# Kernel optimization log

Measured on AMD Instinct MI355X. Metric: run time of the kernel, lower is better.

## Reference

```python
import jax, jax.numpy as jnp
import numpy as np


def _reduce1(x):
    # x: [B, n, d] -> [B, 2d]; exists=max, forall=min over objects (exclude_self is a no-op for cnt=1)
    return jnp.concatenate([x.max(axis=1), x.min(axis=1)], axis=-1)


def _reduce2(x):
    # x: [B, n, n, d] -> [B, n, 2d]; exclude_self masks diagonal i==j (0 for exists/max, 1 for forall/min)
    n = x.shape[1]
    diag = jnp.eye(n, dtype=bool)[None, :, :, None]
    exists = jnp.where(diag, 0.0, x).max(axis=2)
    forall = jnp.where(diag, 1.0, x).min(axis=2)
    return jnp.concatenate([exists, forall], axis=-1)


def _layer(f0, f1, f2, p):
    # One LogicLayer step (breadth=2, minmax reducer, exclude_self, sigmoid norm, no hidden layers)
    W0, b0, W1, b1, W2, b2 = p
    B, n, d1 = f1.shape
    # order 0: [self, reduce(order1)]
    g0 = jnp.concatenate([f0, _reduce1(f1)], axis=-1)
    o0 = jax.nn.sigmoid(g0 @ W0 + b0)
    # order 1: [expand(order0), self, reduce(order2)]
    e0 = jnp.broadcast_to(f0[:, None, :], (B, n, f0.shape[-1]))
    g1 = jnp.concatenate([e0, f1, _reduce2(f2)], axis=-1)
    o1 = jax.nn.sigmoid(g1 @ W1 + b1)
    # order 2: [expand(order1), self] then Permutation(2) = cat(x, swap(i,j))
    e1 = jnp.broadcast_to(f1[:, :, None, :], (B, n, n, d1))
    g2 = jnp.concatenate([e1, f2], axis=-1)
    g2 = jnp.concatenate([g2, jnp.swapaxes(g2, 1, 2)], axis=-1)
    o2 = jax.nn.sigmoid(g2 @ W2 + b2)
    return o0, o1, o2


def setup_inputs() -> dict:
    key = jax.random.key(0)
    B, n = 4, 256
    d = [32, 64, 64]
    O = 128
    ks = iter(jax.random.split(key, 64))
    inp = {
        "x0": jax.random.uniform(next(ks), (B, d[0]), dtype=jnp.float32),
        "x1": jax.random.uniform(next(ks), (B, n, d[1]), dtype=jnp.float32),
        "x2": jax.random.uniform(next(ks), (B, n, n, d[2]), dtype=jnp.float32),
    }
    fan_ins = [
        (d[0] + 2 * d[1], d[0] + d[1] + 2 * d[2], 2 * (d[1] + d[2])),  # layer 0
        (O + 2 * O, O + O + 2 * O, 2 * (O + O)),                        # layer 1
        (O + 2 * O, O + O + 2 * O, 2 * (O + O)),                        # layer 2
    ]
    for l, fins in enumerate(fan_ins):
        for o, fin in enumerate(fins):
            inp[f"W{o}_{l}"] = jax.random.normal(next(ks), (fin, O), dtype=jnp.float32) / np.sqrt(fin).astype(np.float32)
            inp[f"b{o}_{l}"] = jnp.zeros((O,), dtype=jnp.float32)
    return inp


def reference(x0, x1, x2,
              W0_0, b0_0, W1_0, b1_0, W2_0, b2_0,
              W0_1, b0_1, W1_1, b1_1, W2_1, b2_1,
              W0_2, b0_2, W1_2, b1_2, W2_2, b2_2):
    f = (x0, x1, x2)
    for p in ((W0_0, b0_0, W1_0, b1_0, W2_0, b2_0),
              (W0_1, b0_1, W1_1, b1_1, W2_1, b2_1),
              (W0_2, b0_2, W1_2, b1_2, W2_2, b2_2)):
        f = _layer(*f, p)
    return f
```

## Files before the change

### kernel.cpp

```cpp
#include <hip/hip_runtime.h>
#include <hip/hip_bf16.h>
#include <cstdint>

#define NN 256
#define NB 4
#define OC 128

using bf16x8_t = __attribute__((ext_vector_type(8))) __bf16;
using f32x4_t  = __attribute__((ext_vector_type(4))) float;

typedef const __attribute__((address_space(1))) uint8_t* gptr1_t;
typedef __attribute__((address_space(3))) uint8_t* lptr3_t;

__device__ __forceinline__ void async_load16(const void* g, void* l) {
  __builtin_amdgcn_global_load_lds((gptr1_t)g, (lptr3_t)l, 16, 0, 0);
}

__device__ __forceinline__ float sigf(float x) {
  return 1.0f / (1.0f + __expf(-x));
}

__device__ __forceinline__ uint16_t f2bf_rne(float f) {
  uint32_t u = __float_as_uint(f);
  uint32_t r = (u + 0x7fffu + ((u >> 16) & 1u)) >> 16;
  return (uint16_t)r;
}

__device__ __forceinline__ void emit_wt(const float* __restrict__ W2,
                                        uint16_t* __restrict__ Wt, int d1,
                                        int d2, int idx) {
  const int K = 2 * d2;
  const int nn = idx / K, k = idx - nn * K;
  const int row = (k < d2) ? (d1 + k) : (2 * d1 + d2 + (k - d2));
  Wt[idx] = f2bf_rne(W2[row * OC + nn]);
}

__device__ __forceinline__ void emit_bt(const float* __restrict__ W1,
                                        const float* __restrict__ W2,
                                        uint16_t* __restrict__ Bt, int D0,
                                        int D1, int D2, int FIN1, int KP,
                                        int idx) {
  const int n = idx / KP, k = idx - n * KP;
  float val = 0.f;
  if (n < 128) {
    if (k < FIN1) val = W1[k * OC + n];
  } else if (n < 256) {
    if (k >= D0 && k < D0 + D1) val = W2[(k - D0) * OC + (n - 128)];
  } else {
    if (k >= D0 && k < D0 + D1) val = W2[(D1 + D2 + (k - D0)) * OC + (n - 256)];
  }
  Bt[idx] = f2bf_rne(val);
}

__global__ __launch_bounds__(256) void prep_all(
    const float* __restrict__ W2_0, const float* __restrict__ W2_1,
    const float* __restrict__ W2_2, const float* __restrict__ W1_0,
    const float* __restrict__ W1_1, const float* __restrict__ W1_2,
    const float* __restrict__ x0, const float* __restrict__ x1,
    uint16_t* __restrict__ Wt0, uint16_t* __restrict__ Wt1,
    uint16_t* __restrict__ Wt2, uint16_t* __restrict__ Bt0,
    uint16_t* __restrict__ Bt1, uint16_t* __restrict__ Bt2,
    uint16_t* __restrict__ g1bf0, float* __restrict__ r2b,
    float* __restrict__ r2c) {
  int g = blockIdx.x * 256 + threadIdx.x;
  if (g < 16384) { emit_wt(W2_0, Wt0, 64, 64, g); return; }
  g -= 16384;
  if (g < 32768) { emit_wt(W2_1, Wt1, 128, 128, g); return; }
  g -= 32768;
  if (g < 32768) { emit_wt(W2_2, Wt2, 128, 128, g); return; }
  g -= 32768;
  if (g < 98304) { emit_bt(W1_0, W2_0, Bt0, 32, 64, 64, 224, 256, g); return; }
  g -= 98304;
  if (g < 196608) { emit_bt(W1_1, W2_1, Bt1, 128, 128, 128, 512, 512, g); return; }
  g -= 196608;
  if (g < 196608) { emit_bt(W1_2, W2_2, Bt2, 128, 128, 128, 512, 512, g); return; }
  g -= 196608;
  if (g < 131072) {
    const int row = g >> 7, t = g & 127;
    uint16_t* const gp = g1bf0 + (size_t)row * 256;
    if (t < 32) gp[t] = f2bf_rne(x0[(row >> 8) * 32 + t]);
    else if (t < 96) gp[t] = f2bf_rne(x1[(size_t)row * 64 + (t - 32)]);
    else gp[128 + t] = 0;
    return;
  }
  g -= 131072;
  if (g < 262144) { r2b[g] = ((g & 255) < 128) ? 0.f : 1.f; return; }
  g -= 262144;
  if (g < 262144) { r2c[g] = ((g & 255) < 128) ? 0.f : 1.f; }
}

__global__ __launch_bounds__(256) void reduce2_l0_kernel(
    const float* __restrict__ x2, uint16_t* __restrict__ g1bf0,
    uint16_t* __restrict__ x2bf) {
  const int bid = blockIdx.x;
  const int i = bid & 255;
  const int tid = threadIdx.x;
  const int q = tid & 15, s = tid >> 4;
  const size_t rowbase = ((size_t)bid * NN) * 64 + q * 4;
  float mxA0 = 0.f, mxA1 = 0.f, mxA2 = 0.f, mxA3 = 0.f;
  float mnA0 = 1.f, mnA1 = 1.f, mnA2 = 1.f, mnA3 = 1.f;
  float mxB0 = 0.f, mxB1 = 0.f, mxB2 = 0.f, mxB3 = 0.f;
  float mnB0 = 1.f, mnB1 = 1.f, mnB2 = 1.f, mnB3 = 1.f;
#pragma unroll 2
  for (int t = 0; t < 16; t += 2) {
    const int jA = s + t * 16, jB = jA + 16;
    const float4 xa = *(const float4*)(x2 + rowbase + (size_t)jA * 64);
    const float4 xb = *(const float4*)(x2 + rowbase + (size_t)jB * 64);
    uint2 pa, pb;
    pa.x = (uint32_t)f2bf_rne(xa.x) | ((uint32_t)f2bf_rne(xa.y) << 16);
    pa.y = (uint32_t)f2bf_rne(xa.z) | ((uint32_t)f2bf_rne(xa.w) << 16);
    pb.x = (uint32_t)f2bf_rne(xb.x) | ((uint32_t)f2bf_rne(xb.y) << 16);
    pb.y = (uint32_t)f2bf_rne(xb.z) | ((uint32_t)f2bf_rne(xb.w) << 16);
    *(uint2*)(x2bf + rowbase + (size_t)jA * 64) = pa;
    *(uint2*)(x2bf + rowbase + (size_t)jB * 64) = pb;
    if (jA != i) {
      mxA0 = fmaxf(mxA0, xa.x); mxA1 = fmaxf(mxA1, xa.y);
      mxA2 = fmaxf(mxA2, xa.z); mxA3 = fmaxf(mxA3, xa.w);
      mnA0 = fminf(mnA0, xa.x); mnA1 = fminf(mnA1, xa.y);
      mnA2 = fminf(mnA2, xa.z); mnA3 = fminf(mnA3, xa.w);
    }
    if (jB != i) {
      mxB0 = fmaxf(mxB0, xb.x); mxB1 = fmaxf(mxB1, xb.y);
      mxB2 = fmaxf(mxB2, xb.z); mxB3 = fmaxf(mxB3, xb.w);
      mnB0 = fminf(mnB0, xb.x); mnB1 = fminf(mnB1, xb.y);
      mnB2 = fminf(mnB2, xb.z); mnB3 = fminf(mnB3, xb.w);
    }
  }
  float mx0 = fmaxf(mxA0, mxB0), mx1 = fmaxf(mxA1, mxB1);
  float mx2 = fmaxf(mxA2, mxB2), mx3 = fmaxf(mxA3, mxB3);
  float mn0 = fminf(mnA0, mnB0), mn1 = fminf(mnA1, mnB1);
  float mn2 = fminf(mnA2, mnB2), mn3 = fminf(mnA3, mnB3);
  __shared__ float4 smx[256], smn[256];
  smx[tid] = make_float4(mx0, mx1, mx2, mx3);
  smn[tid] = make_float4(mn0, mn1, mn2, mn3);
  __syncthreads();
  if (s == 0) {
    for (int ss = 1; ss < 16; ++ss) {
      float4 a = smx[q + ss * 16], c = smn[q + ss * 16];
      mx0 = fmaxf(mx0, a.x); mx1 = fmaxf(mx1, a.y);
      mx2 = fmaxf(mx2, a.z); mx3 = fmaxf(mx3, a.w);
      mn0 = fminf(mn0, c.x); mn1 = fminf(mn1, c.y);
      mn2 = fminf(mn2, c.z); mn3 = fminf(mn3, c.w);
    }
    uint16_t* const g = g1bf0 + (size_t)bid * 256;
    g[96 + q * 4 + 0] = f2bf_rne(mx0); g[96 + q * 4 + 1] = f2bf_rne(mx1);
    g[96 + q * 4 + 2] = f2bf_rne(mx2); g[96 + q * 4 + 3] = f2bf_rne(mx3);
    g[160 + q * 4 + 0] = f2bf_rne(mn0); g[160 + q * 4 + 1] = f2bf_rne(mn1);
    g[160 + q * 4 + 2] = f2bf_rne(mn2); g[160 + q * 4 + 3] = f2bf_rne(mn3);
  }
}

template <int KP, int D0, int D1, bool DUP>
__global__ __launch_bounds__(256) void small_gemm(
    const uint16_t* __restrict__ g1, const uint16_t* __restrict__ Bt,
    const float* __restrict__ b1, const float* __restrict__ b2,
    float* __restrict__ f1out, uint16_t* __restrict__ g1next,
    float* __restrict__ u, float* __restrict__ vT,
    const float* __restrict__ f0in, const float* __restrict__ f1in,
    const float* __restrict__ W0, const float* __restrict__ b0,
    float* __restrict__ f0out) {
  constexpr int NCH = KP / 64;
  const int bid = blockIdx.x;
  const int tid = threadIdx.x;

  __shared__ __align__(16) uint8_t ldsA[8192];
  __shared__ __align__(16) uint8_t ldsB[16384];

  if (bid < 48) {
    const int mt = bid / 3, nt = bid - mt * 3;
    const int m0 = mt * 64, n0 = nt * 128;
    const int wv = tid >> 6, lane = tid & 63;
    const int l15 = lane & 15, l4 = lane >> 4;

    f32x4_t acc[4][2];
#pragma unroll
    for (int a = 0; a < 4; ++a)
#pragma unroll
      for (int q = 0; q < 2; ++q) acc[a][q] = (f32x4_t){0.f, 0.f, 0.f, 0.f};

    for (int c = 0; c < NCH; ++c) {
      const int kbg = c * 64;
#pragma unroll
      for (int t = 0; t < 2; ++t) {
        const int id = wv * 2 + t;
        const int mi = id & 3, ks = id >> 2;
        async_load16(g1 + (size_t)(m0 + mi * 16 + l15) * KP + kbg + ks * 32 + l4 * 8,
                     ldsA + id * 1024);
      }
#pragma unroll
      for (int t = 0; t < 4; ++t) {
        const int id = wv * 4 + t;
        const int ni = id & 7, ks = id >> 3;
        async_load16(Bt + (size_t)(n0 + ni * 16 + l15) * KP + kbg + ks * 32 + l4 * 8,
                     ldsB + id * 1024);
      }
      __syncthreads();
#pragma unroll
      for (int ks = 0; ks < 2; ++ks) {
        bf16x8_t Af[4], Bf[2];
#pragma unroll
        for (int a = 0; a < 4; ++a)
          Af[a] = *(const bf16x8_t*)(ldsA + ((ks * 4 + a) << 10) + (lane << 4));
#pragma unroll
        for (int q = 0; q < 2; ++q)
          Bf[q] = *(const bf16x8_t*)(ldsB + ((ks * 8 + wv * 2 + q) << 10) + (lane << 4));
#pragma unroll
        for (int a = 0; a < 4; ++a)
#pragma unroll
          for (int q = 0; q < 2; ++q)
            acc[a][q] = __builtin_amdgcn_mfma_f32_16x16x32_bf16(Af[a], Bf[q],
                                                                acc[a][q], 0, 0, 0);
      }
      __syncthreads();
    }

    float bias[2];
#pragma unroll
    for (int q = 0; q < 2; ++q) {
      const int cc = wv * 32 + q * 16 + l15;
      bias[q] = (nt == 0) ? b1[cc] : ((nt == 1) ? b2[cc] : 0.f);
    }
#pragma unroll
    for (int a = 0; a < 4; ++a) {
      const int rl = a * 16 + l4 * 4;
#pragma unroll
      for (int r = 0; r < 4; ++r) {
        const size_t bi = m0 + rl + r;
#pragma unroll
        for (int q = 0; q < 2; ++q) {
          const int cc = wv * 32 + q * 16 + l15;
          const float x = acc[a][q][r] + bias[q];
          if (nt == 0) {
            const float val = sigf(x);
            f1out[bi * OC + cc] = val;
            if (DUP) g1next[bi * 512 + 128 + cc] = f2bf_rne(val);
          } else if (nt == 1) {
            u[bi * OC + cc] = x;
          } else {
            const int b = (int)(bi >> 8), j = (int)(bi & 255);
            vT[((size_t)b * OC + cc) * NN + j] = x;
          }
        }
      }
    }
  } else {
    constexpr int FIN0 = D0 + 2 * D1;
    constexpr int S = 256 / D1;
    const int b = bid - 48;
    float* const sm = (float*)ldsA;
    float* const g0 = sm;
    float* const smx = sm + 512;
    float* const smn = sm + 768;
    float* const sval = sm + 1024;
    const int cc = tid & (D1 - 1), ss = tid / D1;
    float mx = -1e30f, mn = 1e30f;
    const float* f1b = f1in + (size_t)b * NN * D1;
    for (int j = ss; j < NN; j += S) {
      const float x = f1b[(size_t)j * D1 + cc];
      mx = fmaxf(mx, x); mn = fminf(mn, x);
    }
    smx[tid] = mx; smn[tid] = mn;
    __syncthreads();
    if (ss == 0) {
      for (int s2 = 1; s2 < S; ++s2) {
        mx = fmaxf(mx, smx[cc + s2 * D1]);
        mn = fminf(mn, smn[cc + s2 * D1]);
      }
      g0[D0 + cc] = mx;
      g0[D0 + D1 + cc] = mn;
    }
    if (tid < D0) g0[tid] = f0in[b * D0 + tid];
    __syncthreads();
    if (tid < OC) {
      float acc = b0[tid];
#pragma unroll 8
      for (int k = 0; k < FIN0; ++k) acc += g0[k] * W0[k * OC + tid];
      const float val = sigf(acc);
      f0out[b * OC + tid] = val;
      sval[tid] = val;
    }
    if (DUP) {
      __syncthreads();
      for (int idx = tid; idx < 256 * 128; idx += 256) {
        const int row = idx >> 7, c2 = idx & 127;
        g1next[((size_t)(b * 256 + row)) * 512 + c2] = f2bf_rne(sval[c2]);
      }
    }
  }
}

__global__ __launch_bounds__(256) void conv_r2_kernel(
    const float* __restrict__ r2, uint16_t* __restrict__ g1next) {
  const int bi = blockIdx.x, t = threadIdx.x;
  g1next[(size_t)bi * 512 + 256 + t] = f2bf_rne(r2[(size_t)bi * 256 + t]);
}

template <int D2, typename OUT_T, bool REDUCE>
__global__ __launch_bounds__(256, 4) void gemm2_kernel(
    const __hip_bfloat16* __restrict__ f2, const uint16_t* __restrict__ Wt,
    const float* __restrict__ u, const float* __restrict__ vT,
    OUT_T* __restrict__ out, float* __restrict__ r2n) {
  constexpr int K = 2 * D2;
  constexpr int NCH = K / 64;
  constexpr bool BF16OUT = (sizeof(OUT_T) == 2);
  constexpr int LDSB = BF16OUT ? (128 * 272) : 32768;
  const int bid = blockIdx.x;
  const int jt = bid & 1, i = (bid >> 1) & 255, b = bid >> 9;
  const int j0 = jt * 128;
  const int tid = threadIdx.x;
  const int wv = tid >> 6, lane = tid & 63;
  const int wr = wv >> 1, wc = wv & 1;
  const int l15 = lane & 15, l4 = lane >> 4;

  __shared__ __align__(16) uint8_t lds[LDSB];
  __shared__ unsigned smax[128], smin[128];
  uint8_t* const ldsA = lds;
  uint8_t* const ldsW = lds + 16384;

  const __hip_bfloat16* A1 = f2 + ((size_t)(b * NN + i) * NN + j0) * D2;
  const __hip_bfloat16* A2 = f2 + ((size_t)(b * NN + j0) * NN + i) * D2;

  f32x4_t acc[4][4];
#pragma unroll
  for (int a = 0; a < 4; ++a)
#pragma unroll
    for (int q = 0; q < 4; ++q) acc[a][q] = (f32x4_t){0.f, 0.f, 0.f, 0.f};

  for (int c = 0; c < NCH; ++c) {
    const int kbg = c * 64;
    const bool second = (kbg >= D2);
    const __hip_bfloat16* Ab = second ? A2 : A1;
    const size_t rstride = second ? (size_t)NN * D2 : (size_t)D2;
    const int kbase = second ? (kbg - D2) : kbg;
#pragma unroll
    for (int q = 0; q < 4; ++q) {
      const int id = wv * 4 + q;
      const int mi = id & 7, ks = id >> 3;
      const int row = mi * 16 + l15;
      const int kk = ks * 32 + l4 * 8;
      async_load16(Ab + (size_t)row * rstride + kbase + kk, ldsA + id * 1024);
    }
#pragma unroll
    for (int q = 0; q < 4; ++q) {
      const int id = wv * 4 + q;
      const int ni = id & 7, ks = id >> 3;
      const int nn2 = ni * 16 + l15;
      const int kk = ks * 32 + l4 * 8;
      async_load16(Wt + (size_t)nn2 * K + kbg + kk, ldsW + id * 1024);
    }
    __syncthreads();
#pragma unroll
    for (int ks = 0; ks < 2; ++ks) {
      bf16x8_t Af[4], Bf[4];
#pragma unroll
      for (int a = 0; a < 4; ++a)
        Af[a] = *(const bf16x8_t*)(ldsA + ((ks * 8 + wr * 4 + a) << 10) + (lane << 4));
#pragma unroll
      for (int q = 0; q < 4; ++q)
        Bf[q] = *(const bf16x8_t*)(ldsW + ((ks * 8 + wc * 4 + q) << 10) + (lane << 4));
#pragma unroll
      for (int a = 0; a < 4; ++a)
#pragma unroll
        for (int q = 0; q < 4; ++q)
          acc[a][q] = __builtin_amdgcn_mfma_f32_16x16x32_bf16(Af[a], Bf[q],
                                                              acc[a][q], 0, 0, 0);
    }
    __syncthreads();
  }

  const size_t bi2 = (size_t)(b * NN + i);
  float uval[4];
#pragma unroll
  for (int q = 0; q < 4; ++q) uval[q] = u[bi2 * OC + wc * 64 + q * 16 + l15];
  const size_t obase = (bi2 * NN + j0) * OC;
  const float* const vTb = vT + (size_t)b * OC * NN;

  if (BF16OUT) {
    if (REDUCE && tid < 128) { smax[tid] = 0u; smin[tid] = 0x3f800000u; }
    __syncthreads();
    float lmx[4] = {0.f, 0.f, 0.f, 0.f};
    float lmn[4] = {1.f, 1.f, 1.f, 1.f};
#pragma unroll
    for (int a = 0; a < 4; ++a) {
      const int rowb = wr * 64 + a * 16 + l4 * 4;
      const int jg = j0 + rowb;
#pragma unroll
      for (int q = 0; q < 4; ++q) {
        const int col = wc * 64 + q * 16 + l15;
        const float4 vq = *(const float4*)(vTb + (size_t)col * NN + jg);
#pragma unroll
        for (int r = 0; r < 4; ++r) {
          const int j = rowb + r;
          const float x = acc[a][q][r] + uval[q] + ((const float*)&vq)[r];
          const float sg = sigf(x);
          *(uint16_t*)(lds + j * 272 + col * 2) = f2bf_rne(sg);
          if (REDUCE && (jg + r) != i) {
            lmx[q] = fmaxf(lmx[q], sg);
            lmn[q] = fminf(lmn[q], sg);
          }
        }
      }
    }
    if (REDUCE) {
#pragma unroll
      for (int q = 0; q < 4; ++q) {
        const int col = wc * 64 + q * 16 + l15;
        atomicMax(&smax[col], __float_as_uint(lmx[q]));
        atomicMin(&smin[col], __float_as_uint(lmn[q]));
      }
    }
    __syncthreads();
    uint16_t* const outp = (uint16_t*)out;
#pragma unroll
    for (int ci = 0; ci < 8; ++ci) {
      const int chunk = ci * 256 + tid;
      const int row = chunk >> 4, off = chunk & 15;
      const uint4 val = *(const uint4*)(lds + row * 272 + off * 16);
      *(uint4*)(outp + obase + (size_t)row * OC + off * 8) = val;
    }
    if (REDUCE && tid < 128) {
      unsigned* const r2u = (unsigned*)r2n;
      atomicMax(&r2u[bi2 * 256 + tid], smax[tid]);
      atomicMin(&r2u[bi2 * 256 + 128 + tid], smin[tid]);
    }
  } else {
    float* const outp = (float*)out;
#pragma unroll
    for (int a = 0; a < 4; ++a) {
      const int rowb = wr * 64 + a * 16 + l4 * 4;
      const int jg = j0 + rowb;
#pragma unroll
      for (int q = 0; q < 4; ++q) {
        const int col = wc * 64 + q * 16 + l15;
        const float4 vq = *(const float4*)(vTb + (size_t)col * NN + jg);
#pragma unroll
        for (int r = 0; r < 4; ++r) {
          const int j = rowb + r;
          const float x = acc[a][q][r] + uval[q] + ((const float*)&vq)[r];
          outp[obase + (size_t)j * OC + col] = sigf(x);
        }
      }
    }
  }
}

extern "C" void kernel_launch(void* const* d_in, const int* in_sizes, int n_in,
                              void* d_out, int out_size, void* d_ws,
                              size_t ws_size, hipStream_t stream) {
  const float* x0 = (const float*)d_in[0];
  const float* x1 = (const float*)d_in[1];
  const float* x2 = (const float*)d_in[2];
  const float *Wp[3][3], *bp[3][3];
  for (int l = 0; l < 3; ++l)
    for (int o = 0; o < 3; ++o) {
      Wp[l][o] = (const float*)d_in[3 + l * 6 + o * 2];
      bp[l][o] = (const float*)d_in[3 + l * 6 + o * 2 + 1];
    }

  const size_t F2E = (size_t)NB * NN * NN * OC;
  const size_t X2E = (size_t)NB * NN * NN * 64;

  uint8_t* ws = (uint8_t*)d_ws;
  size_t off = 0;
  auto carve = [&](size_t bytes) -> uint8_t* {
    uint8_t* p = ws + off;
    off += (bytes + 255) & ~(size_t)255;
    return p;
  };
  float* f0a = (float*)carve((size_t)NB * OC * 4);
  float* f0b = (float*)carve((size_t)NB * OC * 4);
  float* f1a = (float*)carve((size_t)NB * NN * OC * 4);
  float* f1b = (float*)carve((size_t)NB * NN * OC * 4);
  float* r2b = (float*)carve((size_t)NB * NN * 256 * 4);
  float* r2c = (float*)carve((size_t)NB * NN * 256 * 4);
  float* uu  = (float*)carve((size_t)NB * NN * OC * 4);
  float* vT  = (float*)carve((size_t)NB * OC * NN * 4);
  uint16_t* Wt0 = (uint16_t*)carve((size_t)OC * 128 * 2);
  uint16_t* Wt1 = (uint16_t*)carve((size_t)OC * 256 * 2);
  uint16_t* Wt2 = (uint16_t*)carve((size_t)OC * 256 * 2);
  uint16_t* Bt0 = (uint16_t*)carve((size_t)384 * 256 * 2);
  uint16_t* Bt1 = (uint16_t*)carve((size_t)384 * 512 * 2);
  uint16_t* Bt2 = (uint16_t*)carve((size_t)384 * 512 * 2);
  uint16_t* g1bf0 = (uint16_t*)carve((size_t)NB * NN * 256 * 2);
  uint16_t* g1bf1 = (uint16_t*)carve((size_t)NB * NN * 512 * 2);
  uint16_t* g1bf2 = (uint16_t*)carve((size_t)NB * NN * 512 * 2);
  __hip_bfloat16* f2a = (__hip_bfloat16*)carve(F2E * 2);

  __hip_bfloat16* f2b;
  uint16_t* x2bf;
  if (ws_size >= off + F2E * 2) {
    f2b = (__hip_bfloat16*)carve(F2E * 2);
    x2bf = (uint16_t*)f2b;
  } else {
    f2b = (__hip_bfloat16*)d_in[2];
    x2bf = (uint16_t*)carve(X2E * 2);
  }

  float* out_f0 = (float*)d_out;
  float* out_f1 = out_f0 + (size_t)NB * OC;
  float* out_f2 = out_f1 + (size_t)NB * NN * OC;

  prep_all<<<4800, 256, 0, stream>>>(Wp[0][2], Wp[1][2], Wp[2][2], Wp[0][1],
                                     Wp[1][1], Wp[2][1], x0, x1, Wt0, Wt1, Wt2,
                                     Bt0, Bt1, Bt2, g1bf0, r2b, r2c);
  reduce2_l0_kernel<<<NB * NN, 256, 0, stream>>>(x2, g1bf0, x2bf);

  small_gemm<256, 32, 64, true><<<52, 256, 0, stream>>>(
      g1bf0, Bt0, bp[0][1], bp[0][2], f1a, g1bf1, uu, vT, x0, x1, Wp[0][0],
      bp[0][0], f0a);
  gemm2_kernel<64, __hip_bfloat16, true><<<NB * NN * 2, 256, 0, stream>>>(
      (const __hip_bfloat16*)x2bf, Wt0, uu, vT, f2a, r2b);
  conv_r2_kernel<<<NB * NN, 256, 0, stream>>>(r2b, g1bf1);

  small_gemm<512, 128, 128, true><<<52, 256, 0, stream>>>(
      g1bf1, Bt1, bp[1][1], bp[1][2], f1b, g1bf2, uu, vT, f0a, f1a, Wp[1][0],
      bp[1][0], f0b);
  gemm2_kernel<128, __hip_bfloat16, true><<<NB * NN * 2, 256, 0, stream>>>(
      f2a, Wt1, uu, vT, f2b, r2c);
  conv_r2_kernel<<<NB * NN, 256, 0, stream>>>(r2c, g1bf2);

  small_gemm<512, 128, 128, false><<<52, 256, 0, stream>>>(
      g1bf2, Bt2, bp[2][1], bp[2][2], out_f1, nullptr, uu, vT, f0b, f1b,
      Wp[2][0], bp[2][0], out_f0);
  gemm2_kernel<128, float, false><<<NB * NN * 2, 256, 0, stream>>>(
      f2b, Wt2, uu, vT, out_f2, nullptr);
}
```

Baseline: 518.6 us.

## Load MFMA operands directly from global memory and merge the prep and reduce kernels

New measurement: 569.4 us. 9.8% more time.

```diff
diff --git a/kernel.cpp b/kernel.cpp
--- a/kernel.cpp
+++ b/kernel.cpp
@@ -9,15 +9,8 @@
 using bf16x8_t = __attribute__((ext_vector_type(8))) __bf16;
 using f32x4_t  = __attribute__((ext_vector_type(4))) float;
 
-typedef const __attribute__((address_space(1))) uint8_t* gptr1_t;
-typedef __attribute__((address_space(3))) uint8_t* lptr3_t;
-
-__device__ __forceinline__ void async_load16(const void* g, void* l) {
-  __builtin_amdgcn_global_load_lds((gptr1_t)g, (lptr3_t)l, 16, 0, 0);
-}
-
 __device__ __forceinline__ float sigf(float x) {
-  return 1.0f / (1.0f + __expf(-x));
+  return __builtin_amdgcn_rcpf(1.0f + __expf(-x));
 }
 
 __device__ __forceinline__ uint16_t f2bf_rne(float f) {
@@ -52,7 +45,7 @@
   Bt[idx] = f2bf_rne(val);
 }
 
-__global__ __launch_bounds__(256) void prep_all(
+__global__ __launch_bounds__(256) void prep_reduce(
     const float* __restrict__ W2_0, const float* __restrict__ W2_1,
     const float* __restrict__ W2_2, const float* __restrict__ W1_0,
     const float* __restrict__ W1_1, const float* __restrict__ W1_2,
@@ -61,40 +54,43 @@
     uint16_t* __restrict__ Wt2, uint16_t* __restrict__ Bt0,
     uint16_t* __restrict__ Bt1, uint16_t* __restrict__ Bt2,
     uint16_t* __restrict__ g1bf0, float* __restrict__ r2b,
-    float* __restrict__ r2c) {
-  int g = blockIdx.x * 256 + threadIdx.x;
-  if (g < 16384) { emit_wt(W2_0, Wt0, 64, 64, g); return; }
-  g -= 16384;
-  if (g < 32768) { emit_wt(W2_1, Wt1, 128, 128, g); return; }
-  g -= 32768;
-  if (g < 32768) { emit_wt(W2_2, Wt2, 128, 128, g); return; }
-  g -= 32768;
-  if (g < 98304) { emit_bt(W1_0, W2_0, Bt0, 32, 64, 64, 224, 256, g); return; }
-  g -= 98304;
-  if (g < 196608) { emit_bt(W1_1, W2_1, Bt1, 128, 128, 128, 512, 512, g); return; }
-  g -= 196608;
-  if (g < 196608) { emit_bt(W1_2, W2_2, Bt2, 128, 128, 128, 512, 512, g); return; }
-  g -= 196608;
-  if (g < 131072) {
-    const int row = g >> 7, t = g & 127;
-    uint16_t* const gp = g1bf0 + (size_t)row * 256;
-    if (t < 32) gp[t] = f2bf_rne(x0[(row >> 8) * 32 + t]);
-    else if (t < 96) gp[t] = f2bf_rne(x1[(size_t)row * 64 + (t - 32)]);
-    else gp[128 + t] = 0;
+    float* __restrict__ r2c, const float* __restrict__ x2,
+    uint16_t* __restrict__ x2bf) {
+  __shared__ float4 smx[256], smn[256];
+  const int blk = blockIdx.x;
+  const int tid = threadIdx.x;
+
+  if (blk < 4800) {
+    int g = blk * 256 + tid;
+    if (g < 16384) { emit_wt(W2_0, Wt0, 64, 64, g); return; }
+    g -= 16384;
+    if (g < 32768) { emit_wt(W2_1, Wt1, 128, 128, g); return; }
+    g -= 32768;
+    if (g < 32768) { emit_wt(W2_2, Wt2, 128, 128, g); return; }
+    g -= 32768;
+    if (g < 98304) { emit_bt(W1_0, W2_0, Bt0, 32, 64, 64, 224, 256, g); return; }
+    g -= 98304;
+    if (g < 196608) { emit_bt(W1_1, W2_1, Bt1, 128, 128, 128, 512, 512, g); return; }
+    g -= 196608;
+    if (g < 196608) { emit_bt(W1_2, W2_2, Bt2, 128, 128, 128, 512, 512, g); return; }
+    g -= 196608;
+    if (g < 131072) {
+      const int row = g >> 7, t = g & 127;
+      uint16_t* const gp = g1bf0 + (size_t)row * 256;
+      if (t < 32) gp[t] = f2bf_rne(x0[(row >> 8) * 32 + t]);
+      else if (t < 96) gp[t] = f2bf_rne(x1[(size_t)row * 64 + (t - 32)]);
+      else gp[128 + t] = 0;
+      return;
+    }
+    g -= 131072;
+    if (g < 262144) { r2b[g] = ((g & 255) < 128) ? 0.f : 1.f; return; }
+    g -= 262144;
+    if (g < 262144) { r2c[g] = ((g & 255) < 128) ? 0.f : 1.f; }
     return;
   }
-  g -= 131072;
-  if (g < 262144) { r2b[g] = ((g & 255) < 128) ? 0.f : 1.f; return; }
-  g -= 262144;
-  if (g < 262144) { r2c[g] = ((g & 255) < 128) ? 0.f : 1.f; }
-}
-
-__global__ __launch_bounds__(256) void reduce2_l0_kernel(
-    const float* __restrict__ x2, uint16_t* __restrict__ g1bf0,
-    uint16_t* __restrict__ x2bf) {
-  const int bid = blockIdx.x;
+
+  const int bid = blk - 4800;
   const int i = bid & 255;
-  const int tid = threadIdx.x;
   const int q = tid & 15, s = tid >> 4;
   const size_t rowbase = ((size_t)bid * NN) * 64 + q * 4;
   float mxA0 = 0.f, mxA1 = 0.f, mxA2 = 0.f, mxA3 = 0.f;
@@ -130,7 +126,6 @@
   float mx2 = fmaxf(mxA2, mxB2), mx3 = fmaxf(mxA3, mxB3);
   float mn0 = fminf(mnA0, mnB0), mn1 = fminf(mnA1, mnB1);
   float mn2 = fminf(mnA2, mnB2), mn3 = fminf(mnA3, mnB3);
-  __shared__ float4 smx[256], smn[256];
   smx[tid] = make_float4(mx0, mx1, mx2, mx3);
   smn[tid] = make_float4(mn0, mn1, mn2, mn3);
   __syncthreads();
@@ -159,12 +154,9 @@
     const float* __restrict__ f0in, const float* __restrict__ f1in,
     const float* __restrict__ W0, const float* __restrict__ b0,
     float* __restrict__ f0out) {
-  constexpr int NCH = KP / 64;
   const int bid = blockIdx.x;
   const int tid = threadIdx.x;
-
-  __shared__ __align__(16) uint8_t ldsA[8192];
-  __shared__ __align__(16) uint8_t ldsB[16384];
+  __shared__ float sm[1280];
 
   if (bid < 48) {
     const int mt = bid / 3, nt = bid - mt * 3;
@@ -172,46 +164,37 @@
     const int wv = tid >> 6, lane = tid & 63;
     const int l15 = lane & 15, l4 = lane >> 4;
 
+    const uint16_t* const Ag = g1 + (size_t)m0 * KP;
+    const uint16_t* const Bg = Bt + (size_t)n0 * KP;
+    uint32_t offA[4], offB[2];
+#pragma unroll
+    for (int a = 0; a < 4; ++a)
+      offA[a] = (uint32_t)(a * 16 + l15) * KP + l4 * 8;
+#pragma unroll
+    for (int q = 0; q < 2; ++q)
+      offB[q] = (uint32_t)(wv * 32 + q * 16 + l15) * KP + l4 * 8;
+
     f32x4_t acc[4][2];
 #pragma unroll
     for (int a = 0; a < 4; ++a)
 #pragma unroll
       for (int q = 0; q < 2; ++q) acc[a][q] = (f32x4_t){0.f, 0.f, 0.f, 0.f};
 
-    for (int c = 0; c < NCH; ++c) {
-      const int kbg = c * 64;
-#pragma unroll
-      for (int t = 0; t < 2; ++t) {
-        const int id = wv * 2 + t;
-        const int mi = id & 3, ks = id >> 2;
-        async_load16(g1 + (size_t)(m0 + mi * 16 + l15) * KP + kbg + ks * 32 + l4 * 8,
-                     ldsA + id * 1024);
-      }
-#pragma unroll
-      for (int t = 0; t < 4; ++t) {
-        const int id = wv * 4 + t;
-        const int ni = id & 7, ks = id >> 3;
-        async_load16(Bt + (size_t)(n0 + ni * 16 + l15) * KP + kbg + ks * 32 + l4 * 8,
-                     ldsB + id * 1024);
-      }
-      __syncthreads();
-#pragma unroll
-      for (int ks = 0; ks < 2; ++ks) {
-        bf16x8_t Af[4], Bf[2];
-#pragma unroll
-        for (int a = 0; a < 4; ++a)
-          Af[a] = *(const bf16x8_t*)(ldsA + ((ks * 4 + a) << 10) + (lane << 4));
+#pragma unroll
+    for (int kb = 0; kb < KP; kb += 32) {
+      bf16x8_t Af[4], Bf[2];
+#pragma unroll
+      for (int a = 0; a < 4; ++a)
+        Af[a] = *(const bf16x8_t*)(Ag + offA[a] + kb);
+#pragma unroll
+      for (int q = 0; q < 2; ++q)
+        Bf[q] = *(const bf16x8_t*)(Bg + offB[q] + kb);
+#pragma unroll
+      for (int a = 0; a < 4; ++a)
 #pragma unroll
         for (int q = 0; q < 2; ++q)
-          Bf[q] = *(const bf16x8_t*)(ldsB + ((ks * 8 + wv * 2 + q) << 10) + (lane << 4));
-#pragma unroll
-        for (int a = 0; a < 4; ++a)
-#pragma unroll
-          for (int q = 0; q < 2; ++q)
-            acc[a][q] = __builtin_amdgcn_mfma_f32_16x16x32_bf16(Af[a], Bf[q],
-                                                                acc[a][q], 0, 0, 0);
-      }
-      __syncthreads();
+          acc[a][q] = __builtin_amdgcn_mfma_f32_16x16x32_bf16(Af[a], Bf[q],
+                                                              acc[a][q], 0, 0, 0);
     }
 
     float bias[2];
@@ -247,7 +230,6 @@
     constexpr int FIN0 = D0 + 2 * D1;
     constexpr int S = 256 / D1;
     const int b = bid - 48;
-    float* const sm = (float*)ldsA;
     float* const g0 = sm;
     float* const smx = sm + 512;
     float* const smn = sm + 768;
@@ -301,9 +283,8 @@
     const float* __restrict__ u, const float* __restrict__ vT,
     OUT_T* __restrict__ out, float* __restrict__ r2n) {
   constexpr int K = 2 * D2;
-  constexpr int NCH = K / 64;
   constexpr bool BF16OUT = (sizeof(OUT_T) == 2);
-  constexpr int LDSB = BF16OUT ? (128 * 272) : 32768;
+  constexpr int LDSB = BF16OUT ? (128 * 272) : 16;
   const int bid = blockIdx.x;
   const int jt = bid & 1, i = (bid >> 1) & 255, b = bid >> 9;
   const int j0 = jt * 128;
@@ -314,11 +295,21 @@
 
   __shared__ __align__(16) uint8_t lds[LDSB];
   __shared__ unsigned smax[128], smin[128];
-  uint8_t* const ldsA = lds;
-  uint8_t* const ldsW = lds + 16384;
-
-  const __hip_bfloat16* A1 = f2 + ((size_t)(b * NN + i) * NN + j0) * D2;
-  const __hip_bfloat16* A2 = f2 + ((size_t)(b * NN + j0) * NN + i) * D2;
+
+  const __hip_bfloat16* const A1 = f2 + ((size_t)(b * NN + i) * NN + j0) * D2;
+  const __hip_bfloat16* const A2 = f2 + ((size_t)(b * NN + j0) * NN + i) * D2;
+  const __hip_bfloat16* const Wg = (const __hip_bfloat16*)Wt;
+
+  uint32_t offA1[4], offA2[4], offW[4];
+#pragma unroll
+  for (int a = 0; a < 4; ++a) {
+    const uint32_t row = wr * 64 + a * 16 + l15;
+    offA1[a] = row * (uint32_t)D2 + l4 * 8;
+    offA2[a] = row * (uint32_t)(NN * D2) + l4 * 8;
+  }
+#pragma unroll
+  for (int q = 0; q < 4; ++q)
+    offW[q] = (uint32_t)(wc * 64 + q * 16 + l15) * K + l4 * 8;
 
   f32x4_t acc[4][4];
 #pragma unroll
@@ -326,46 +317,27 @@
 #pragma unroll
     for (int q = 0; q < 4; ++q) acc[a][q] = (f32x4_t){0.f, 0.f, 0.f, 0.f};
 
-  for (int c = 0; c < NCH; ++c) {
-    const int kbg = c * 64;
-    const bool second = (kbg >= D2);
-    const __hip_bfloat16* Ab = second ? A2 : A1;
-    const size_t rstride = second ? (size_t)NN * D2 : (size_t)D2;
-    const int kbase = second ? (kbg - D2) : kbg;
-#pragma unroll
-    for (int q = 0; q < 4; ++q) {
-      const int id = wv * 4 + q;
-      const int mi = id & 7, ks = id >> 3;
-      const int row = mi * 16 + l15;
-      const int kk = ks * 32 + l4 * 8;
-      async_load16(Ab + (size_t)row * rstride + kbase + kk, ldsA + id * 1024);
-    }
-#pragma unroll
-    for (int q = 0; q < 4; ++q) {
-      const int id = wv * 4 + q;
-      const int ni = id & 7, ks = id >> 3;
-      const int nn2 = ni * 16 + l15;
-      const int kk = ks * 32 + l4 * 8;
-      async_load16(Wt + (size_t)nn2 * K + kbg + kk, ldsW + id * 1024);
-    }
-    __syncthreads();
-#pragma unroll
-    for (int ks = 0; ks < 2; ++ks) {
-      bf16x8_t Af[4], Bf[4];
+#pragma unroll
+  for (int kb = 0; kb < K; kb += 32) {
+    bf16x8_t Af[4], Bf[4];
+    if (kb < D2) {
 #pragma unroll
       for (int a = 0; a < 4; ++a)
-        Af[a] = *(const bf16x8_t*)(ldsA + ((ks * 8 + wr * 4 + a) << 10) + (lane << 4));
+        Af[a] = *(const bf16x8_t*)(A1 + offA1[a] + kb);
+    } else {
+#pragma unroll
+      for (int a = 0; a < 4; ++a)
+        Af[a] = *(const bf16x8_t*)(A2 + offA2[a] + (kb - D2));
+    }
+#pragma unroll
+    for (int q = 0; q < 4; ++q)
+      Bf[q] = *(const bf16x8_t*)(Wg + offW[q] + kb);
+#pragma unroll
+    for (int a = 0; a < 4; ++a)
 #pragma unroll
       for (int q = 0; q < 4; ++q)
-        Bf[q] = *(const bf16x8_t*)(ldsW + ((ks * 8 + wc * 4 + q) << 10) + (lane << 4));
-#pragma unroll
-      for (int a = 0; a < 4; ++a)
-#pragma unroll
-        for (int q = 0; q < 4; ++q)
-          acc[a][q] = __builtin_amdgcn_mfma_f32_16x16x32_bf16(Af[a], Bf[q],
-                                                              acc[a][q], 0, 0, 0);
-    }
-    __syncthreads();
+        acc[a][q] = __builtin_amdgcn_mfma_f32_16x16x32_bf16(Af[a], Bf[q],
+                                                            acc[a][q], 0, 0, 0);
   }
 
   const size_t bi2 = (size_t)(b * NN + i);
@@ -500,10 +472,9 @@
   float* out_f1 = out_f0 + (size_t)NB * OC;
   float* out_f2 = out_f1 + (size_t)NB * NN * OC;
 
-  prep_all<<<4800, 256, 0, stream>>>(Wp[0][2], Wp[1][2], Wp[2][2], Wp[0][1],
-                                     Wp[1][1], Wp[2][1], x0, x1, Wt0, Wt1, Wt2,
-                                     Bt0, Bt1, Bt2, g1bf0, r2b, r2c);
-  reduce2_l0_kernel<<<NB * NN, 256, 0, stream>>>(x2, g1bf0, x2bf);
+  prep_reduce<<<4800 + NB * NN, 256, 0, stream>>>(
+      Wp[0][2], Wp[1][2], Wp[2][2], Wp[0][1], Wp[1][1], Wp[2][1], x0, x1, Wt0,
+      Wt1, Wt2, Bt0, Bt1, Bt2, g1bf0, r2b, r2c, x2, x2bf);
 
   small_gemm<256, 32, 64, true><<<52, 256, 0, stream>>>(
       g1bf0, Bt0, bp[0][1], bp[0][2], f1a, g1bf1, uu, vT, x0, x1, Wp[0][0],
```

## Double-buffer gemm2 K-loop and merge prep and layer-0 reduce kernels

Applied to the files above, without the earlier changes.

Result: no change. 514.1 us (-0.9%).

```diff
diff --git a/kernel.cpp b/kernel.cpp
--- a/kernel.cpp
+++ b/kernel.cpp
@@ -17,7 +17,7 @@
 }
 
 __device__ __forceinline__ float sigf(float x) {
-  return 1.0f / (1.0f + __expf(-x));
+  return __builtin_amdgcn_rcpf(1.0f + __expf(-x));
 }
 
 __device__ __forceinline__ uint16_t f2bf_rne(float f) {
@@ -52,7 +52,7 @@
   Bt[idx] = f2bf_rne(val);
 }
 
-__global__ __launch_bounds__(256) void prep_all(
+__global__ __launch_bounds__(256) void prep_reduce(
     const float* __restrict__ W2_0, const float* __restrict__ W2_1,
     const float* __restrict__ W2_2, const float* __restrict__ W1_0,
     const float* __restrict__ W1_1, const float* __restrict__ W1_2,
@@ -61,40 +61,43 @@
     uint16_t* __restrict__ Wt2, uint16_t* __restrict__ Bt0,
     uint16_t* __restrict__ Bt1, uint16_t* __restrict__ Bt2,
     uint16_t* __restrict__ g1bf0, float* __restrict__ r2b,
-    float* __restrict__ r2c) {
-  int g = blockIdx.x * 256 + threadIdx.x;
-  if (g < 16384) { emit_wt(W2_0, Wt0, 64, 64, g); return; }
-  g -= 16384;
-  if (g < 32768) { emit_wt(W2_1, Wt1, 128, 128, g); return; }
-  g -= 32768;
-  if (g < 32768) { emit_wt(W2_2, Wt2, 128, 128, g); return; }
-  g -= 32768;
-  if (g < 98304) { emit_bt(W1_0, W2_0, Bt0, 32, 64, 64, 224, 256, g); return; }
-  g -= 98304;
-  if (g < 196608) { emit_bt(W1_1, W2_1, Bt1, 128, 128, 128, 512, 512, g); return; }
-  g -= 196608;
-  if (g < 196608) { emit_bt(W1_2, W2_2, Bt2, 128, 128, 128, 512, 512, g); return; }
-  g -= 196608;
-  if (g < 131072) {
-    const int row = g >> 7, t = g & 127;
-    uint16_t* const gp = g1bf0 + (size_t)row * 256;
-    if (t < 32) gp[t] = f2bf_rne(x0[(row >> 8) * 32 + t]);
-    else if (t < 96) gp[t] = f2bf_rne(x1[(size_t)row * 64 + (t - 32)]);
-    else gp[128 + t] = 0;
+    float* __restrict__ r2c, const float* __restrict__ x2,
+    uint16_t* __restrict__ x2bf) {
+  __shared__ float4 smx[256], smn[256];
+  const int blk = blockIdx.x;
+  const int tid = threadIdx.x;
+
+  if (blk < 4800) {
+    int g = blk * 256 + tid;
+    if (g < 16384) { emit_wt(W2_0, Wt0, 64, 64, g); return; }
+    g -= 16384;
+    if (g < 32768) { emit_wt(W2_1, Wt1, 128, 128, g); return; }
+    g -= 32768;
+    if (g < 32768) { emit_wt(W2_2, Wt2, 128, 128, g); return; }
+    g -= 32768;
+    if (g < 98304) { emit_bt(W1_0, W2_0, Bt0, 32, 64, 64, 224, 256, g); return; }
+    g -= 98304;
+    if (g < 196608) { emit_bt(W1_1, W2_1, Bt1, 128, 128, 128, 512, 512, g); return; }
+    g -= 196608;
+    if (g < 196608) { emit_bt(W1_2, W2_2, Bt2, 128, 128, 128, 512, 512, g); return; }
+    g -= 196608;
+    if (g < 131072) {
+      const int row = g >> 7, t = g & 127;
+      uint16_t* const gp = g1bf0 + (size_t)row * 256;
+      if (t < 32) gp[t] = f2bf_rne(x0[(row >> 8) * 32 + t]);
+      else if (t < 96) gp[t] = f2bf_rne(x1[(size_t)row * 64 + (t - 32)]);
+      else gp[128 + t] = 0;
+      return;
+    }
+    g -= 131072;
+    if (g < 262144) { r2b[g] = ((g & 255) < 128) ? 0.f : 1.f; return; }
+    g -= 262144;
+    if (g < 262144) { r2c[g] = ((g & 255) < 128) ? 0.f : 1.f; }
     return;
   }
-  g -= 131072;
-  if (g < 262144) { r2b[g] = ((g & 255) < 128) ? 0.f : 1.f; return; }
-  g -= 262144;
-  if (g < 262144) { r2c[g] = ((g & 255) < 128) ? 0.f : 1.f; }
-}
-
-__global__ __launch_bounds__(256) void reduce2_l0_kernel(
-    const float* __restrict__ x2, uint16_t* __restrict__ g1bf0,
-    uint16_t* __restrict__ x2bf) {
-  const int bid = blockIdx.x;
+
+  const int bid = blk - 4800;
   const int i = bid & 255;
-  const int tid = threadIdx.x;
   const int q = tid & 15, s = tid >> 4;
   const size_t rowbase = ((size_t)bid * NN) * 64 + q * 4;
   float mxA0 = 0.f, mxA1 = 0.f, mxA2 = 0.f, mxA3 = 0.f;
@@ -130,7 +133,6 @@
   float mx2 = fmaxf(mxA2, mxB2), mx3 = fmaxf(mxA3, mxB3);
   float mn0 = fminf(mnA0, mnB0), mn1 = fminf(mnA1, mnB1);
   float mn2 = fminf(mnA2, mnB2), mn3 = fminf(mnA3, mnB3);
-  __shared__ float4 smx[256], smn[256];
   smx[tid] = make_float4(mx0, mx1, mx2, mx3);
   smn[tid] = make_float4(mn0, mn1, mn2, mn3);
   __syncthreads();
@@ -301,7 +303,7 @@
     const float* __restrict__ u, const float* __restrict__ vT,
     OUT_T* __restrict__ out, float* __restrict__ r2n) {
   constexpr int K = 2 * D2;
-  constexpr int NCH = K / 64;
+  constexpr int NCH = K / 32;
   constexpr bool BF16OUT = (sizeof(OUT_T) == 2);
   constexpr int LDSB = BF16OUT ? (128 * 272) : 32768;
   const int bid = blockIdx.x;
@@ -314,11 +316,9 @@
 
   __shared__ __align__(16) uint8_t lds[LDSB];
   __shared__ unsigned smax[128], smin[128];
-  uint8_t* const ldsA = lds;
-  uint8_t* const ldsW = lds + 16384;
-
-  const __hip_bfloat16* A1 = f2 + ((size_t)(b * NN + i) * NN + j0) * D2;
-  const __hip_bfloat16* A2 = f2 + ((size_t)(b * NN + j0) * NN + i) * D2;
+
+  const __hip_bfloat16* const A1 = f2 + ((size_t)(b * NN + i) * NN + j0) * D2;
+  const __hip_bfloat16* const A2 = f2 + ((size_t)(b * NN + j0) * NN + i) * D2;
 
   f32x4_t acc[4][4];
 #pragma unroll
@@ -326,47 +326,66 @@
 #pragma unroll
     for (int q = 0; q < 4; ++q) acc[a][q] = (f32x4_t){0.f, 0.f, 0.f, 0.f};
 
-  for (int c = 0; c < NCH; ++c) {
-    const int kbg = c * 64;
+  auto STAGE = [&](int c, int buf) {
+    const int kbg = c * 32;
+    uint8_t* const bA = lds + buf * 16384;
+    uint8_t* const bW = bA + 8192;
     const bool second = (kbg >= D2);
-    const __hip_bfloat16* Ab = second ? A2 : A1;
+    const __hip_bfloat16* const Ab = second ? A2 : A1;
     const size_t rstride = second ? (size_t)NN * D2 : (size_t)D2;
     const int kbase = second ? (kbg - D2) : kbg;
 #pragma unroll
-    for (int q = 0; q < 4; ++q) {
-      const int id = wv * 4 + q;
-      const int mi = id & 7, ks = id >> 3;
-      const int row = mi * 16 + l15;
-      const int kk = ks * 32 + l4 * 8;
-      async_load16(Ab + (size_t)row * rstride + kbase + kk, ldsA + id * 1024);
-    }
-#pragma unroll
-    for (int q = 0; q < 4; ++q) {
-      const int id = wv * 4 + q;
-      const int ni = id & 7, ks = id >> 3;
-      const int nn2 = ni * 16 + l15;
-      const int kk = ks * 32 + l4 * 8;
-      async_load16(Wt + (size_t)nn2 * K + kbg + kk, ldsW + id * 1024);
-    }
-    __syncthreads();
-#pragma unroll
-    for (int ks = 0; ks < 2; ++ks) {
-      bf16x8_t Af[4], Bf[4];
-#pragma unroll
-      for (int a = 0; a < 4; ++a)
-        Af[a] = *(const bf16x8_t*)(ldsA + ((ks * 8 + wr * 4 + a) << 10) + (lane << 4));
+    for (int t = 0; t < 2; ++t) {
+      const int mi = wv * 2 + t;
+      async_load16(Ab + (size_t)(mi * 16 + l15) * rstride + kbase + l4 * 8,
+                   bA + mi * 1024);
+    }
+#pragma unroll
+    for (int t = 0; t < 2; ++t) {
+      const int ni = wv * 2 + t;
+      async_load16(Wt + (size_t)(ni * 16 + l15) * K + kbg + l4 * 8,
+                   bW + ni * 1024);
+    }
+  };
+
+  auto COMPUTE = [&](int buf) {
+    const uint8_t* const bA = lds + buf * 16384;
+    const uint8_t* const bW = bA + 8192;
+    bf16x8_t Af[4], Bf[4];
+#pragma unroll
+    for (int a = 0; a < 4; ++a)
+      Af[a] = *(const bf16x8_t*)(bA + ((wr * 4 + a) << 10) + (lane << 4));
+#pragma unroll
+    for (int q = 0; q < 4; ++q)
+      Bf[q] = *(const bf16x8_t*)(bW + ((wc * 4 + q) << 10) + (lane << 4));
+#pragma unroll
+    for (int a = 0; a < 4; ++a)
 #pragma unroll
       for (int q = 0; q < 4; ++q)
-        Bf[q] = *(const bf16x8_t*)(ldsW + ((ks * 8 + wc * 4 + q) << 10) + (lane << 4));
-#pragma unroll
-      for (int a = 0; a < 4; ++a)
-#pragma unroll
-        for (int q = 0; q < 4; ++q)
-          acc[a][q] = __builtin_amdgcn_mfma_f32_16x16x32_bf16(Af[a], Bf[q],
-                                                              acc[a][q], 0, 0, 0);
-    }
-    __syncthreads();
-  }
+        acc[a][q] = __builtin_amdgcn_mfma_f32_16x16x32_bf16(Af[a], Bf[q],
+                                                            acc[a][q], 0, 0, 0);
+  };
+
+  STAGE(0, 0);
+#pragma unroll
+  for (int c = 0; c < NCH - 1; ++c) {
+    STAGE(c + 1, (c + 1) & 1);
+    asm volatile("s_waitcnt vmcnt(4)" ::: "memory");
+    __builtin_amdgcn_sched_barrier(0);
+    __builtin_amdgcn_s_barrier();
+    __builtin_amdgcn_sched_barrier(0);
+    COMPUTE(c & 1);
+    asm volatile("s_waitcnt lgkmcnt(0)" ::: "memory");
+    __builtin_amdgcn_sched_barrier(0);
+    __builtin_amdgcn_s_barrier();
+    __builtin_amdgcn_sched_barrier(0);
+  }
+  asm volatile("s_waitcnt vmcnt(0)" ::: "memory");
+  __builtin_amdgcn_sched_barrier(0);
+  __builtin_amdgcn_s_barrier();
+  __builtin_amdgcn_sched_barrier(0);
+  COMPUTE((NCH - 1) & 1);
+  __syncthreads();
 
   const size_t bi2 = (size_t)(b * NN + i);
   float uval[4];
@@ -500,10 +519,9 @@
   float* out_f1 = out_f0 + (size_t)NB * OC;
   float* out_f2 = out_f1 + (size_t)NB * NN * OC;
 
-  prep_all<<<4800, 256, 0, stream>>>(Wp[0][2], Wp[1][2], Wp[2][2], Wp[0][1],
-                                     Wp[1][1], Wp[2][1], x0, x1, Wt0, Wt1, Wt2,
-                                     Bt0, Bt1, Bt2, g1bf0, r2b, r2c);
-  reduce2_l0_kernel<<<NB * NN, 256, 0, stream>>>(x2, g1bf0, x2bf);
+  prep_reduce<<<4800 + NB * NN, 256, 0, stream>>>(
+      Wp[0][2], Wp[1][2], Wp[2][2], Wp[0][1], Wp[1][1], Wp[2][1], x0, x1, Wt0,
+      Wt1, Wt2, Bt0, Bt1, Bt2, g1bf0, r2b, r2c, x2, x2bf);
 
   small_gemm<256, 32, 64, true><<<52, 256, 0, stream>>>(
       g1bf0, Bt0, bp[0][1], bp[0][2], f1a, g1bf1, uu, vT, x0, x1, Wp[0][0],
```
